# Optimization experiments

Hardware: AMD Instinct MI355X
Metric: run time of the kernel (lower is better)

Reference implementation:

```python
import jax, jax.numpy as jnp
import numpy as np
from jax.scipy.linalg import solve_triangular

EPS = 1e-5
CHUNK = 64

def _rms(x, w, eps=EPS):
    return x * jax.lax.rsqrt(jnp.mean(x * x, axis=-1, keepdims=True) + eps) * w

def _l2norm(x, eps=1e-6):
    return x * jax.lax.rsqrt(jnp.sum(x * x, axis=-1, keepdims=True) + eps)

def _causal_conv(x, w):
    # x: [B,T,C], w: [C,K] depthwise causal short conv
    K = w.shape[1]
    T = x.shape[1]
    xp = jnp.pad(x, ((0, 0), (K - 1, 0), (0, 0)))
    return sum(xp[:, j:j + T, :] * w[:, j] for j in range(K))

def _chunk_gated_delta_rule(q, k, v, g, beta, chunk=CHUNK):
    # q,k: [B,H,T,Dk] (l2-normalized, q pre-scaled); v: [B,H,T,Dv]; g,beta: [B,H,T]
    Bb, H, T, Dk = k.shape
    Dv = v.shape[-1]
    N = T // chunk
    qc, kc, vc = (a.reshape(Bb, H, N, chunk, -1) for a in (q, k, v))
    gc = g.reshape(Bb, H, N, chunk)
    bc = beta.reshape(Bb, H, N, chunk)
    gcs = jnp.cumsum(gc, axis=-1)  # within-chunk cumulative log-decay
    tri = jnp.tril(jnp.ones((chunk, chunk), bool))
    tri_s = jnp.tril(jnp.ones((chunk, chunk), bool), -1)
    diff = gcs[..., :, None] - gcs[..., None, :]
    decay = jnp.where(tri, jnp.exp(jnp.where(tri, diff, 0.0)), 0.0)  # [B,H,N,C,C]
    k_beta = kc * bc[..., None]
    v_beta = vc * bc[..., None]
    A = jnp.einsum('bhnck,bhndk->bhncd', k_beta, kc) * decay
    A = jnp.where(tri_s, A, 0.0)
    eye = jnp.eye(chunk, dtype=q.dtype)
    Tmat = solve_triangular(eye + A, jnp.broadcast_to(eye, A.shape), lower=True)  # (I+A)^-1
    u = Tmat @ v_beta                               # [B,H,N,C,Dv]
    w = Tmat @ (k_beta * jnp.exp(gcs)[..., None])   # [B,H,N,C,Dk]

    def step(S, inp):
        q_i, k_i, u_i, w_i, g_i, dm_i = inp
        attn = jnp.where(tri, jnp.einsum('bhck,bhdk->bhcd', q_i, k_i) * dm_i, 0.0)
        v_new = u_i - w_i @ S
        o_i = (q_i * jnp.exp(g_i)[..., None]) @ S + attn @ v_new
        g_last = g_i[..., -1]
        k_dec = k_i * jnp.exp(g_last[..., None] - g_i)[..., None]
        S = S * jnp.exp(g_last)[..., None, None] + jnp.einsum('bhck,bhcv->bhkv', k_dec, v_new)
        return S, o_i

    xs = tuple(jnp.moveaxis(a, 2, 0) for a in (qc, kc, u, w, gcs, decay))
    S0 = jnp.zeros((Bb, H, Dk, Dv), q.dtype)
    _, outs = jax.lax.scan(step, S0, xs)  # [N,B,H,C,Dv]
    return jnp.moveaxis(outs, 0, 2).reshape(Bb, H, T, Dv)

def _layer_forward(x, mask, ln1_w, qkvz_w, ba_w, conv_w, A_log, dt_bias,
                   o_norm_w, out_w, ln2_w, gate_w, up_w, down_w):
    B, T, D = x.shape
    H = A_log.shape[0]
    kd = qkvz_w.shape[0] // 4  # key_dim == value_dim here (k_heads==v_heads, Dk==Dv)
    vd = kd
    Dk = kd // H
    Dv = vd // H
    silu = jax.nn.silu
    h = _rms(x, ln1_w)
    qkvz = h @ qkvz_w.T
    q, k, v, z = jnp.split(qkvz, [kd, 2 * kd, 2 * kd + vd], axis=-1)
    b, a = jnp.split(h @ ba_w.T, 2, axis=-1)  # [B,T,H] each
    mixed = jnp.concatenate([q, k, v], axis=-1) * mask[..., None]
    mixed = silu(_causal_conv(mixed, conv_w))
    q, k, v = jnp.split(mixed, [kd, 2 * kd], axis=-1)
    q = _l2norm(q.reshape(B, T, H, Dk))
    k = _l2norm(k.reshape(B, T, H, Dk))
    v = v.reshape(B, T, H, Dv)
    beta = jax.nn.sigmoid(b) * mask[..., None]
    g = -jnp.exp(A_log) * jax.nn.softplus(a + dt_bias) * mask[..., None]
    scale = Dk ** -0.5
    bhtd = lambda t: jnp.transpose(t, (0, 2, 1, 3))
    o = _chunk_gated_delta_rule(bhtd(q) * scale, bhtd(k), bhtd(v),
                                jnp.transpose(g, (0, 2, 1)), jnp.transpose(beta, (0, 2, 1)))
    o = jnp.transpose(o, (0, 2, 1, 3))  # [B,T,H,Dv]
    o = _rms(o, o_norm_w) * silu(z.reshape(B, T, H, Dv))  # gated RMSNorm
    x = x + o.reshape(B, T, vd) @ out_w.T
    h2 = _rms(x, ln2_w)
    mlp_out = (silu(h2 @ gate_w.T) * (h2 @ up_w.T)) @ down_w.T
    return x + mlp_out

def setup_inputs():
    key = jax.random.key(0)
    ks = jax.random.split(key, 12)
    B, T, D, H, Dk, Dv, M, K = 1, 4096, 2048, 16, 128, 128, 8192, 4
    kd, vd = H * Dk, H * Dv
    nrm = lambda i, shp, sc=0.02: jax.random.normal(ks[i], shp, jnp.float32) * sc
    return {
        'x': nrm(0, (B, T, D), 1.0),
        'mask': jnp.ones((B, T), jnp.float32),
        'ln1_w': jnp.ones((D,), jnp.float32),
        'qkvz_w': nrm(1, (2 * kd + 2 * vd, D)),
        'ba_w': nrm(2, (2 * H, D)),
        'conv_w': nrm(3, (2 * kd + vd, K), 0.3),
        'A_log': jnp.log(jax.random.uniform(ks[4], (H,), jnp.float32, 1.0, 16.0)),
        'dt_bias': nrm(5, (H,), 0.5),
        'o_norm_w': jnp.ones((Dv,), jnp.float32),
        'out_w': nrm(6, (D, vd)),
        'ln2_w': jnp.ones((D,), jnp.float32),
        'gate_w': nrm(7, (M, D)),
        'up_w': nrm(8, (M, D)),
        'down_w': nrm(9, (D, M)),
    }

def reference(x, mask, ln1_w, qkvz_w, ba_w, conv_w, A_log, dt_bias,
              o_norm_w, out_w, ln2_w, gate_w, up_w, down_w):
    return _layer_forward(x, mask, ln1_w, qkvz_w, ba_w, conv_w, A_log, dt_bias,
                          o_norm_w, out_w, ln2_w, gate_w, up_w, down_w)
```

## Files before the change

kernel.cpp:

```cpp
#include <hip/hip_runtime.h>
#include <math.h>

#define T_LEN 4096
#define DMODEL 2048
#define NH 16
#define CQKV 6144
#define CQKVZ 8192
#define SCALE 0.08838834764831845f

using bf16x8 = __attribute__((ext_vector_type(8))) short;
using f32x4  = __attribute__((ext_vector_type(4))) float;

__device__ __forceinline__ float siluf(float x) { return x / (1.0f + __expf(-x)); }

__device__ __forceinline__ unsigned short f2bf(float f) {
  unsigned int u = __float_as_uint(f);
  u = (u + 0x7FFFu + ((u >> 16) & 1u)) >> 16;
  return (unsigned short)u;
}
__device__ __forceinline__ float bf2f(unsigned short u) {
  return __uint_as_float(((unsigned int)u) << 16);
}
__device__ __forceinline__ ushort4 pack4(float a, float b, float c, float d) {
  ushort4 r; r.x = f2bf(a); r.y = f2bf(b); r.z = f2bf(c); r.w = f2bf(d); return r;
}

__device__ __forceinline__ void gl_lds16(const unsigned short* g, unsigned short* l) {
  __builtin_amdgcn_global_load_lds(
      (const __attribute__((address_space(1))) void*)g,
      (__attribute__((address_space(3))) void*)l, 16, 0, 0);
}

template<int MODE>
__global__ __launch_bounds__(256) void rmsnorm_kernel(const float* __restrict__ x,
                                                      const float* __restrict__ w,
                                                      float* __restrict__ outf,
                                                      unsigned short* __restrict__ outb) {
  const int t = blockIdx.x;
  const int tid = threadIdx.x;
  const float4* xr = (const float4*)(x + (size_t)t * DMODEL);
  float4 v0 = xr[tid];
  float4 v1 = xr[tid + 256];
  float s = v0.x*v0.x + v0.y*v0.y + v0.z*v0.z + v0.w*v0.w
          + v1.x*v1.x + v1.y*v1.y + v1.z*v1.z + v1.w*v1.w;
#pragma unroll
  for (int off = 32; off > 0; off >>= 1) s += __shfl_down(s, off);
  __shared__ float red[4];
  if ((tid & 63) == 0) red[tid >> 6] = s;
  __syncthreads();
  const float tot = red[0] + red[1] + red[2] + red[3];
  const float r = rsqrtf(tot * (1.0f / DMODEL) + 1e-5f);
  const float4* wr = (const float4*)w;
  const float4 w0 = wr[tid], w1 = wr[tid + 256];
  float4 o0, o1;
  o0.x = v0.x*r*w0.x; o0.y = v0.y*r*w0.y; o0.z = v0.z*r*w0.z; o0.w = v0.w*r*w0.w;
  o1.x = v1.x*r*w1.x; o1.y = v1.y*r*w1.y; o1.z = v1.z*r*w1.z; o1.w = v1.w*r*w1.w;
  if (MODE == 1) {
    float4* orow = (float4*)(outf + (size_t)t * DMODEL);
    orow[tid] = o0;
    orow[tid + 256] = o1;
  }
  ushort4* brow = (ushort4*)(outb + (size_t)t * DMODEL);
  brow[tid] = pack4(o0.x, o0.y, o0.z, o0.w);
  brow[tid + 256] = pack4(o1.x, o1.y, o1.z, o1.w);
}

__global__ __launch_bounds__(256) void f2b_kernel(const float* __restrict__ in,
                                                  unsigned short* __restrict__ out) {
  const size_t i = (size_t)blockIdx.x * 256 + threadIdx.x;
  const float4 a = ((const float4*)in)[2 * i];
  const float4 b = ((const float4*)in)[2 * i + 1];
  ((ushort4*)out)[2 * i] = pack4(a.x, a.y, a.z, a.w);
  ((ushort4*)out)[2 * i + 1] = pack4(b.x, b.y, b.z, b.w);
}

template<int EPI, int BM>
__global__ __launch_bounds__(512, 1) void gemm256_kernel(const unsigned short* __restrict__ A,
                                                         const unsigned short* __restrict__ B,
                                                         float* __restrict__ Cf,
                                                         unsigned short* __restrict__ Cb,
                                                         int M, int N, int K) {
  constexpr int BN = 256;
  constexpr int MI = BM / 32;
  constexpr int AW = BM / 128;
  __shared__ __align__(16) unsigned short lds[3][(BM + BN) * 32];
  const int nbm = M / BM, nbn = N / BN, nwg = nbm * nbn;
  const int nt = K >> 5;
  int bmi, bni;
  {
    const int bid = blockIdx.x;
    const int cpx = nwg >> 3;
    int sc = 1;
    while (sc * sc < cpx) sc <<= 1;
    if (sc * sc > cpx) sc >>= 1;
    const int scn = (sc > 0) ? (cpx / sc) : 0;
    if ((nwg & 7) == 0 && sc > 0 && sc * scn == cpx && (nbm % sc) == 0 && (nbn % scn) == 0) {
      const int chunk = bid & 7, widx = bid >> 3;
      const int regc = nbn / scn;
      bmi = (chunk / regc) * sc + widx / scn;
      bni = (chunk % regc) * scn + widx % scn;
    } else {
      bmi = bid / nbn; bni = bid % nbn;
    }
  }
  const int bm = bmi * BM, bn = bni * BN;
  const int tid = threadIdx.x;
  const int wv = tid >> 6, ln = tid & 63;
  const int fr = ln & 15, qq = ln >> 4;
  const int wm = wv >> 2, wn = wv & 3;
  const int ra0 = wm * (BM / 2), rb0 = wn * 64;
  const int lrow = ln >> 2;
  const int lslot = ln & 3;

  f32x4 acc[MI][4];
  const f32x4 zero = {0.f, 0.f, 0.f, 0.f};
#pragma unroll
  for (int mi = 0; mi < MI; mi++)
#pragma unroll
    for (int ni = 0; ni < 4; ni++) acc[mi][ni] = zero;

  auto stageA = [&](int buf, int t) {
    const int k0 = t << 5;
#pragma unroll
    for (int q = 0; q < AW; q++) {
      const int lr = q * 128 + wv * 16 + lrow;
      const int sl = lslot ^ ((lr >> 1) & 3);
      gl_lds16(A + (size_t)(bm + lr) * K + k0 + sl * 8,
               &lds[buf][(q * 128 + wv * 16) * 32]);
    }
  };
  auto stageB = [&](int buf, int t) {
    const int k0 = t << 5;
#pragma unroll
    for (int q = 0; q < 2; q++) {
      const int lr = q * 128 + wv * 16 + lrow;
      const int sl = lslot ^ ((lr >> 1) & 3);
      gl_lds16(B + (size_t)(bn + lr) * K + k0 + sl * 8,
               &lds[buf][BM * 32 + (q * 128 + wv * 16) * 32]);
    }
  };

  stageA(0, 0); stageB(0, 0);
  stageA(1, 1); stageB(1, 1);
  if constexpr (AW == 2) asm volatile("s_waitcnt vmcnt(4)" ::: "memory");
  else                   asm volatile("s_waitcnt vmcnt(3)" ::: "memory");
  __builtin_amdgcn_s_barrier();
  asm volatile("" ::: "memory");

  for (int t = 0; t < nt; t++) {
    const int cb = t % 3;
    const int b2 = (t + 2) % 3;
    const unsigned short* lA = &lds[cb][0];
    const unsigned short* lB = &lds[cb][BM * 32];
    bf16x8 bfr[4];
#pragma unroll
    for (int ni = 0; ni < 4; ni++) {
      const int r = rb0 + ni * 16 + fr;
      bfr[ni] = *(const bf16x8*)&lB[r * 32 + ((qq ^ ((r >> 1) & 3)) << 3)];
    }
    bf16x8 afr[MI];
#pragma unroll
    for (int mi = 0; mi < MI; mi++) {
      const int r = ra0 + mi * 16 + fr;
      afr[mi] = *(const bf16x8*)&lA[r * 32 + ((qq ^ ((r >> 1) & 3)) << 3)];
    }
    if (t + 2 < nt) { stageA(b2, t + 2); stageB(b2, t + 2); }
    __builtin_amdgcn_s_setprio(1);
#pragma unroll
    for (int mi = 0; mi < MI; mi++)
#pragma unroll
      for (int ni = 0; ni < 4; ni++)
        acc[mi][ni] = __builtin_amdgcn_mfma_f32_16x16x32_bf16(afr[mi], bfr[ni], acc[mi][ni], 0, 0, 0);
    __builtin_amdgcn_s_setprio(0);
    if (t + 1 < nt) {
      asm volatile("s_waitcnt lgkmcnt(0)" ::: "memory");
      if (t + 2 < nt) {
        if constexpr (AW == 2) asm volatile("s_waitcnt vmcnt(4)" ::: "memory");
        else                   asm volatile("s_waitcnt vmcnt(3)" ::: "memory");
      } else {
        asm volatile("s_waitcnt vmcnt(0)" ::: "memory");
      }
      __builtin_amdgcn_s_barrier();
      asm volatile("" ::: "memory");
    }
  }

  const int cm4 = qq * 4;
#pragma unroll
  for (int mi = 0; mi < MI; mi++) {
#pragma unroll
    for (int ni = 0; ni < 4; ni++) {
#pragma unroll
      for (int r = 0; r < 4; r++) {
        const int grow = bm + ra0 + mi * 16 + cm4 + r;
        const int gcol = bn + rb0 + ni * 16 + fr;
        const size_t off = (size_t)grow * N + gcol;
        const float v = acc[mi][ni][r];
        if (EPI == 0) {
          Cb[off] = f2bf(v);
        } else if (EPI == 1) {
          Cf[off] += v;
        } else {
          Cb[off] = f2bf(siluf(bf2f(Cb[off])) * v);
        }
      }
    }
  }
}

__global__ __launch_bounds__(256) void ba_gemm_kernel(const float* __restrict__ h_in,
                                                      const float* __restrict__ ba_w,
                                                      float* __restrict__ ba_out) {
  __shared__ __align__(16) float hl[2048];
  __shared__ float red[32][9];
  const int t = blockIdx.x;
  const int tid = threadIdx.x;
  const float4* hr = (const float4*)(h_in + (size_t)t * DMODEL);
  ((float4*)hl)[tid] = hr[tid];
  ((float4*)hl)[tid + 256] = hr[tid + 256];
  __syncthreads();
  const int c = tid & 31;
  const int p = tid >> 5;
  const float* wrow = ba_w + (size_t)c * DMODEL + p * 256;
  const float* hrow = hl + p * 256;
  float s = 0.f;
#pragma unroll 8
  for (int k = 0; k < 256; k++) s += hrow[k] * wrow[k];
  red[c][p] = s;
  __syncthreads();
  if (tid < 32) {
    float tot = 0.f;
#pragma unroll
    for (int q = 0; q < 8; q++) tot += red[tid][q];
    ba_out[(size_t)t * 32 + tid] = tot;
  }
}

__global__ __launch_bounds__(256) void zcopy_kernel(const unsigned short* __restrict__ qkvz,
                                                    unsigned short* __restrict__ z) {
  const int idx = blockIdx.x * 256 + threadIdx.x;
  const int t = idx >> 8;
  const int c8 = (idx & 255) * 8;
  *(uint4*)(z + (size_t)t * 2048 + c8) =
      *(const uint4*)(qkvz + (size_t)t * CQKVZ + CQKV + c8);
}

__global__ __launch_bounds__(256) void conv_silu_kernel(const unsigned short* __restrict__ qkvz,
                                                        const float* __restrict__ conv_w,
                                                        const float* __restrict__ mask,
                                                        float* __restrict__ mixed) {
  const int idx = blockIdx.x * 256 + threadIdx.x;
  const int c4 = (idx % 1536) * 4;
  const int t = idx / 1536;
  const float4 w0 = *(const float4*)(conv_w + (size_t)c4 * 4);
  const float4 w1 = *(const float4*)(conv_w + (size_t)c4 * 4 + 4);
  const float4 w2 = *(const float4*)(conv_w + (size_t)c4 * 4 + 8);
  const float4 w3 = *(const float4*)(conv_w + (size_t)c4 * 4 + 12);
  const float wj0[4] = {w0.x, w0.y, w0.z, w0.w};
  const float wj1[4] = {w1.x, w1.y, w1.z, w1.w};
  const float wj2[4] = {w2.x, w2.y, w2.z, w2.w};
  const float wj3[4] = {w3.x, w3.y, w3.z, w3.w};
  float4 acc = make_float4(0.f, 0.f, 0.f, 0.f);
#pragma unroll
  for (int j = 0; j < 4; j++) {
    const int tt = t - 3 + j;
    if (tt < 0) continue;
    const float m = mask[tt];
    const ushort4 xb = *(const ushort4*)(qkvz + (size_t)tt * CQKVZ + c4);
    acc.x += bf2f(xb.x) * m * wj0[j];
    acc.y += bf2f(xb.y) * m * wj1[j];
    acc.z += bf2f(xb.z) * m * wj2[j];
    acc.w += bf2f(xb.w) * m * wj3[j];
  }
  acc.x = siluf(acc.x); acc.y = siluf(acc.y); acc.z = siluf(acc.z); acc.w = siluf(acc.w);
  *(float4*)(mixed + (size_t)t * CQKV + c4) = acc;
}

__global__ __launch_bounds__(256) void l2norm_kernel(float* __restrict__ mixed) {
  const int r = blockIdx.x * 4 + (threadIdx.x >> 6);
  const int lane = threadIdx.x & 63;
  const int t = r >> 5;
  const int hh = r & 31;
  float* p = mixed + (size_t)t * CQKV + hh * 128 + lane * 2;
  float2 v = *(float2*)p;
  float s = v.x * v.x + v.y * v.y;
#pragma unroll
  for (int off = 32; off > 0; off >>= 1) s += __shfl_down(s, off);
  s = __shfl(s, 0);
  const float rn = rsqrtf(s + 1e-6f);
  v.x *= rn; v.y *= rn;
  *(float2*)p = v;
}

__global__ __launch_bounds__(256) void beta_g_kernel(const float* __restrict__ ba,
                                                     const float* __restrict__ A_log,
                                                     const float* __restrict__ dt_bias,
                                                     const float* __restrict__ mask,
                                                     float* __restrict__ beta,
                                                     float* __restrict__ g) {
  const int idx = blockIdx.x * 256 + threadIdx.x;
  const int t = idx >> 4;
  const int h = idx & 15;
  const float b = ba[(size_t)t * 32 + h];
  const float a = ba[(size_t)t * 32 + 16 + h];
  const float m = mask[t];
  beta[idx] = m / (1.0f + expf(-b));
  const float xx = a + dt_bias[h];
  const float sp = (xx > 20.0f) ? xx : log1pf(expf(xx));
  g[idx] = -expf(A_log[h]) * sp * m;
}

__global__ __launch_bounds__(256) void gcs_kernel(const float* __restrict__ g,
                                                  float* __restrict__ gcsbuf,
                                                  float* __restrict__ edkbuf,
                                                  float* __restrict__ egqbuf,
                                                  float* __restrict__ adecbuf) {
  const int idx = blockIdx.x * 256 + threadIdx.x;
  if (idx >= 1024) return;
  const int h = idx >> 6;
  const int n = idx & 63;
  const int t0 = n * 64;
  float s = 0.f;
  for (int i = 0; i < 64; i++) {
    s += g[(size_t)(t0 + i) * NH + h];
    gcsbuf[(size_t)idx * 64 + i] = s;
  }
  const float glast = s;
  adecbuf[idx] = __expf(glast);
  for (int i = 0; i < 64; i++) {
    const float gi = gcsbuf[(size_t)idx * 64 + i];
    edkbuf[(size_t)idx * 64 + i] = __expf(glast - gi);
    egqbuf[(size_t)idx * 64 + i] = __expf(gi) * SCALE;
  }
}

__global__ __launch_bounds__(256) void pre_attn_kernel(const float* __restrict__ mixed,
                                                       const float* __restrict__ gcsbuf,
                                                       const float* __restrict__ betabuf,
                                                       float* __restrict__ abuf,
                                                       float* __restrict__ attnbuf) {
  __shared__ __align__(16) float kl[64][132];
  __shared__ float gcs_s[64];
  __shared__ float betal[64];
  const int blk = blockIdx.x;
  const int h = blk >> 6;
  const int n = blk & 63;
  const int t0 = n * 64;
  const int tid = threadIdx.x;
  if (tid < 64) {
    gcs_s[tid] = gcsbuf[(size_t)blk * 64 + tid];
    betal[tid] = betabuf[(size_t)(t0 + tid) * NH + h];
  }
#pragma unroll
  for (int rep = 0; rep < 8; rep++) {
    const int lin = rep * 256 + tid;
    const int i = lin >> 5;
    const int d = (lin & 31) * 4;
    const float4 kv = *(const float4*)(mixed + (size_t)(t0 + i) * CQKV + 2048 + h * 128 + d);
    *(float4*)&kl[i][d] = kv;
  }
  __syncthreads();
  const int cj = tid & 15;
  const int ri = tid >> 4;
  const int i0 = ri * 4, j0 = cj * 4;
  float accA[4][4], accQ[4][4];
#pragma unroll
  for (int a = 0; a < 4; a++)
#pragma unroll
    for (int b = 0; b < 4; b++) { accA[a][b] = 0.f; accQ[a][b] = 0.f; }
  const float* qbase = mixed + (size_t)t0 * CQKV + h * 128;
#pragma unroll 4
  for (int d = 0; d < 128; d++) {
    const float kj0 = kl[j0][d], kj1 = kl[j0 + 1][d], kj2 = kl[j0 + 2][d], kj3 = kl[j0 + 3][d];
#pragma unroll
    for (int a = 0; a < 4; a++) {
      const float ka = kl[i0 + a][d];
      const float qa = qbase[(size_t)(i0 + a) * CQKV + d];
      accA[a][0] += ka * kj0; accA[a][1] += ka * kj1; accA[a][2] += ka * kj2; accA[a][3] += ka * kj3;
      accQ[a][0] += qa * kj0; accQ[a][1] += qa * kj1; accQ[a][2] += qa * kj2; accQ[a][3] += qa * kj3;
    }
  }
#pragma unroll
  for (int a = 0; a < 4; a++) {
    const int i = i0 + a;
    const float gi = gcs_s[i];
    const float bi = betal[i];
    float4 Av, Qv;
    float dec;
    dec = __expf(fminf(gi - gcs_s[j0 + 0], 0.f));
    Av.x = (i > j0 + 0) ? accA[a][0] * bi * dec : 0.f;
    Qv.x = (i >= j0 + 0) ? accQ[a][0] * dec * SCALE : 0.f;
    dec = __expf(fminf(gi - gcs_s[j0 + 1], 0.f));
    Av.y = (i > j0 + 1) ? accA[a][1] * bi * dec : 0.f;
    Qv.y = (i >= j0 + 1) ? accQ[a][1] * dec * SCALE : 0.f;
    dec = __expf(fminf(gi - gcs_s[j0 + 2], 0.f));
    Av.z = (i > j0 + 2) ? accA[a][2] * bi * dec : 0.f;
    Qv.z = (i >= j0 + 2) ? accQ[a][2] * dec * SCALE : 0.f;
    dec = __expf(fminf(gi - gcs_s[j0 + 3], 0.f));
    Av.w = (i > j0 + 3) ? accA[a][3] * bi * dec : 0.f;
    Qv.w = (i >= j0 + 3) ? accQ[a][3] * dec * SCALE : 0.f;
    *(float4*)(abuf + (size_t)blk * 4096 + i * 64 + j0) = Av;
    *(float4*)(attnbuf + (size_t)blk * 4096 + i * 64 + j0) = Qv;
  }
}

__global__ __launch_bounds__(256) void pre_solve_kernel(const float* __restrict__ abuf,
                                                        const float* __restrict__ betabuf,
                                                        float* __restrict__ tbuf) {
  __shared__ float Al[64][65];
  __shared__ float Tl[64][65];
  const int blk = blockIdx.x;
  const int h = blk >> 6;
  const int n = blk & 63;
  const int t0 = n * 64;
  const int tid = threadIdx.x;
#pragma unroll
  for (int rep = 0; rep < 4; rep++) {
    const int lin = rep * 256 + tid;
    const int i = lin >> 4;
    const int j = (lin & 15) * 4;
    const float4 av = *(const float4*)(abuf + (size_t)blk * 4096 + i * 64 + j);
    Al[i][j] = av.x; Al[i][j + 1] = av.y; Al[i][j + 2] = av.z; Al[i][j + 3] = av.w;
  }
  __syncthreads();
  if (tid < 64) {
    const int j = tid;
    const float bj = betabuf[(size_t)(t0 + j) * NH + h];
    for (int i = 0; i < 64; i++) {
      float s = (i == j) ? 1.0f : 0.0f;
      for (int l = j; l < i; l++) s -= Al[i][l] * Tl[l][j];
      Tl[i][j] = s;
    }
    for (int i = j; i < 64; i++) Tl[i][j] *= bj;
  }
  __syncthreads();
#pragma unroll
  for (int rep = 0; rep < 4; rep++) {
    const int lin = rep * 256 + tid;
    const int i = lin >> 4;
    const int j = (lin & 15) * 4;
    float4 tv;
    tv.x = Tl[i][j]; tv.y = Tl[i][j + 1]; tv.z = Tl[i][j + 2]; tv.w = Tl[i][j + 3];
    *(float4*)(tbuf + (size_t)blk * 4096 + i * 64 + j) = tv;
  }
}

__global__ __launch_bounds__(256) void pre_uw_kernel(const float* __restrict__ mixed,
                                                     const float* __restrict__ tbuf,
                                                     const float* __restrict__ gcsbuf,
                                                     float* __restrict__ ubuf,
                                                     unsigned short* __restrict__ wbf) {
  __shared__ __align__(16) float Tl[64][68];
  __shared__ __align__(16) float xl[64][132];
  __shared__ float egcs[64];
  const int blk = blockIdx.x;
  const int h = blk >> 6;
  const int n = blk & 63;
  const int t0 = n * 64;
  const int tid = threadIdx.x;
  if (tid < 64) egcs[tid] = __expf(gcsbuf[(size_t)blk * 64 + tid]);
#pragma unroll
  for (int rep = 0; rep < 4; rep++) {
    const int lin = rep * 256 + tid;
    const int i = lin >> 4;
    const int j = (lin & 15) * 4;
    const float4 tv = *(const float4*)(tbuf + (size_t)blk * 4096 + i * 64 + j);
    *(float4*)&Tl[i][j] = tv;
  }
#pragma unroll
  for (int rep = 0; rep < 8; rep++) {
    const int lin = rep * 256 + tid;
    const int i = lin >> 5;
    const int d = (lin & 31) * 4;
    const float4 vv = *(const float4*)(mixed + (size_t)(t0 + i) * CQKV + 4096 + h * 128 + d);
    *(float4*)&xl[i][d] = vv;
  }
  __syncthreads();
  const int cgu = tid & 15;
  const int riu = tid >> 4;
  const int i0 = riu * 4;
  const int d0 = cgu * 8;
  float acc[4][8];
#pragma unroll
  for (int a = 0; a < 4; a++)
#pragma unroll
    for (int b = 0; b < 8; b++) acc[a][b] = 0.f;
#pragma unroll 2
  for (int j = 0; j < 64; j++) {
    const float tv[4] = {Tl[i0][j], Tl[i0 + 1][j], Tl[i0 + 2][j], Tl[i0 + 3][j]};
    const float4 x0 = *(const float4*)&xl[j][d0];
    const float4 x1 = *(const float4*)&xl[j][d0 + 4];
    const float xv[8] = {x0.x, x0.y, x0.z, x0.w, x1.x, x1.y, x1.z, x1.w};
#pragma unroll
    for (int a = 0; a < 4; a++)
#pragma unroll
      for (int b = 0; b < 8; b++) acc[a][b] += tv[a] * xv[b];
  }
#pragma unroll
  for (int b = 0; b < 8; b++) {
    *(float4*)(ubuf + (size_t)blk * 8192 + riu * 512 + (size_t)(d0 + b) * 4) =
        make_float4(acc[0][b], acc[1][b], acc[2][b], acc[3][b]);
  }
  __syncthreads();
#pragma unroll
  for (int rep = 0; rep < 8; rep++) {
    const int lin = rep * 256 + tid;
    const int i = lin >> 5;
    const int d = (lin & 31) * 4;
    float4 kv = *(const float4*)(mixed + (size_t)(t0 + i) * CQKV + 2048 + h * 128 + d);
    const float e = egcs[i];
    kv.x *= e; kv.y *= e; kv.z *= e; kv.w *= e;
    *(float4*)&xl[i][d] = kv;
  }
  __syncthreads();
#pragma unroll
  for (int a = 0; a < 4; a++)
#pragma unroll
    for (int b = 0; b < 8; b++) acc[a][b] = 0.f;
#pragma unroll 2
  for (int j = 0; j < 64; j++) {
    const float tv[4] = {Tl[i0][j], Tl[i0 + 1][j], Tl[i0 + 2][j], Tl[i0 + 3][j]};
    const float4 x0 = *(const float4*)&xl[j][d0];
    const float4 x1 = *(const float4*)&xl[j][d0 + 4];
    const float xv[8] = {x0.x, x0.y, x0.z, x0.w, x1.x, x1.y, x1.z, x1.w};
#pragma unroll
    for (int a = 0; a < 4; a++)
#pragma unroll
      for (int b = 0; b < 8; b++) acc[a][b] += tv[a] * xv[b];
  }
#pragma unroll
  for (int a = 0; a < 4; a++) {
    const int l = i0 + a;
    unsigned short* wp = wbf + (size_t)(t0 + l) * 2048 + h * 128 + ((cgu ^ (l & 7)) << 3);
    *(ushort4*)wp = pack4(-acc[a][0], -acc[a][1], -acc[a][2], -acc[a][3]);
    *(ushort4*)(wp + 4) = pack4(-acc[a][4], -acc[a][5], -acc[a][6], -acc[a][7]);
  }
}

__global__ __launch_bounds__(256) void ktrans_kernel(const float* __restrict__ mixed,
                                                     const float* __restrict__ edkbuf,
                                                     const float* __restrict__ egqbuf,
                                                     unsigned short* __restrict__ kdT,
                                                     unsigned short* __restrict__ qe) {
  __shared__ __align__(16) float kl[64][132];
  __shared__ float edk_s[64];
  __shared__ float egq_s[64];
  const int blk = blockIdx.x;
  const int h = blk >> 6;
  const int n = blk & 63;
  const int t0 = n * 64;
  const int tid = threadIdx.x;
  if (tid < 64) {
    edk_s[tid] = edkbuf[(size_t)blk * 64 + tid];
    egq_s[tid] = egqbuf[(size_t)blk * 64 + tid];
  }
#pragma unroll
  for (int q = 0; q < 8; q++) {
    const int idx = tid + q * 256;
    const int l = idx >> 5, c4 = (idx & 31) * 4;
    *(float4*)&kl[l][c4] = *(const float4*)(mixed + (size_t)(t0 + l) * CQKV + 2048 + h * 128 + c4);
  }
  __syncthreads();
#pragma unroll
  for (int q = 0; q < 4; q++) {
    const int idx = tid + q * 256;
    const int d = idx >> 3, lsl = idx & 7;
    const int l8 = lsl * 8;
    float v[8];
#pragma unroll
    for (int j = 0; j < 8; j++) v[j] = kl[l8 + j][d] * edk_s[l8 + j];
    unsigned short* p = kdT + (size_t)blk * 8192 + d * 64 + ((lsl ^ (d & 7)) << 3);
    *(ushort4*)p = pack4(v[0], v[1], v[2], v[3]);
    *(ushort4*)(p + 4) = pack4(v[4], v[5], v[6], v[7]);
  }
#pragma unroll
  for (int q = 0; q < 8; q++) {
    const int idx = tid + q * 256;
    const int i = idx >> 5, c4 = (idx & 31) * 4;
    const float4 v = *(const float4*)(mixed + (size_t)(t0 + i) * CQKV + h * 128 + c4);
    const float e = egq_s[i];
    *(ushort4*)(qe + (size_t)(t0 + i) * 2048 + h * 128 + c4) =
        pack4(v.x * e, v.y * e, v.z * e, v.w * e);
  }
}

__global__ __launch_bounds__(512, 1) void scan_kernel(const unsigned short* __restrict__ wbf,
                                                      const unsigned short* __restrict__ kdT,
                                                      const float* __restrict__ ubuf,
                                                      const float* __restrict__ adecbuf,
                                                      unsigned short* __restrict__ STb,
                                                      unsigned short* __restrict__ vtb,
                                                      const float* __restrict__ gw,
                                                      const float* __restrict__ uw,
                                                      const float* __restrict__ dw,
                                                      const float* __restrict__ ow,
                                                      const float* __restrict__ xin,
                                                      unsigned short* __restrict__ Wg,
                                                      unsigned short* __restrict__ Wu,
                                                      unsigned short* __restrict__ Wd,
                                                      unsigned short* __restrict__ Wo,
                                                      float* __restrict__ outc) {
  __shared__ __align__(16) unsigned short stage[2][16384];
  __shared__ __align__(16) unsigned short privAll[8][3072];
  if (blockIdx.x >= 16) {
    const int xb = blockIdx.x - 16;
    const int tid = threadIdx.x;
    if (xb < 13312) {
      const float* src; unsigned short* dst; size_t u;
      if (xb < 4096)       { src = gw; dst = Wg; u = (size_t)xb * 512 + tid; }
      else if (xb < 8192)  { src = uw; dst = Wu; u = (size_t)(xb - 4096) * 512 + tid; }
      else if (xb < 12288) { src = dw; dst = Wd; u = (size_t)(xb - 8192) * 512 + tid; }
      else                 { src = ow; dst = Wo; u = (size_t)(xb - 12288) * 512 + tid; }
      const float4 a = ((const float4*)src)[2 * u];
      const float4 b = ((const float4*)src)[2 * u + 1];
      ((ushort4*)dst)[2 * u] = pack4(a.x, a.y, a.z, a.w);
      ((ushort4*)dst)[2 * u + 1] = pack4(b.x, b.y, b.z, b.w);
    } else {
      const size_t i = (size_t)(xb - 13312) * 512 + tid;
      ((float4*)outc)[2 * i] = ((const float4*)xin)[2 * i];
      ((float4*)outc)[2 * i + 1] = ((const float4*)xin)[2 * i + 1];
    }
    return;
  }
  const int h = blockIdx.x;
  const int tid = threadIdx.x;
  const int ln = tid & 63;
  const int wv = tid >> 6;
  const int fr = ln & 15;
  const int g  = ln >> 4;
  const int c0 = wv * 16;
  const int fsw = fr & 7;
  unsigned short* privA = &privAll[wv][0];
  unsigned short* privB = &privAll[wv][2048];
  const f32x4 zero = {0.f, 0.f, 0.f, 0.f};

  f32x4 acc2[8];
#pragma unroll
  for (int dt = 0; dt < 8; dt++) acc2[dt] = zero;

  auto stage_wk = [&](int buf, int n1) {
    const int t0n = n1 * 64;
    const size_t kbase = (size_t)(h * 64 + n1) * 8192;
#pragma unroll
    for (int q = 0; q < 2; q++) {
      const int m = wv * 2 + q;
      gl_lds16(wbf + (size_t)(t0n + m * 4 + (ln >> 4)) * 2048 + h * 128 + (ln & 15) * 8,
               &stage[buf][m * 512]);
      gl_lds16(kdT + kbase + (m * 8 + (ln >> 3)) * 64 + (ln & 7) * 8,
               &stage[buf][8192 + m * 512]);
    }
  };

  float4 ur4[4];
#pragma unroll
  for (int lt = 0; lt < 4; lt++)
    ur4[lt] = *(const float4*)(ubuf + (size_t)(h * 64) * 8192 + (lt * 4 + g) * 512 + (c0 + fr) * 4);
  float ad = adecbuf[h * 64];
  stage_wk(0, 0);
  asm volatile("s_waitcnt vmcnt(0)" ::: "memory");
  __builtin_amdgcn_s_barrier();
  asm volatile("" ::: "memory");

  for (int n = 0; n < 64; n++) {
    const int blk = h * 64 + n;
    const unsigned short* wl = &stage[n & 1][0];
    const unsigned short* kl = &stage[n & 1][8192];
    if (n + 1 < 64) stage_wk((n + 1) & 1, n + 1);
    __builtin_amdgcn_sched_barrier(0);
    float4 ur4n[4];
    float adn = 0.f;
    if (n + 1 < 64) {
      const size_t ub = (size_t)(blk + 1) * 8192;
#pragma unroll
      for (int lt = 0; lt < 4; lt++)
        ur4n[lt] = *(const float4*)(ubuf + ub + (lt * 4 + g) * 512 + (c0 + fr) * 4);
      adn = adecbuf[blk + 1];
    } else {
      const float4 z4 = make_float4(0.f, 0.f, 0.f, 0.f);
#pragma unroll
      for (int lt = 0; lt < 4; lt++) ur4n[lt] = z4;
    }
    __builtin_amdgcn_sched_barrier(0);
#pragma unroll
    for (int dt = 0; dt < 8; dt++) {
      const int slot = dt * 2 + (g >> 1);
      const ushort4 pv = pack4(acc2[dt][0], acc2[dt][1], acc2[dt][2], acc2[dt][3]);
      *(ushort4*)&privA[fr * 128 + ((slot ^ fsw) << 3) + (g & 1) * 4] = pv;
      *(ushort4*)(STb + (size_t)blk * 16384 + (dt * 4 + g) * 512 + (c0 + fr) * 4) = pv;
    }
    f32x4 acc1[4];
#pragma unroll
    for (int lt = 0; lt < 4; lt++) {
      f32x4 t;
      t[0] = ur4[lt].x; t[1] = ur4[lt].y; t[2] = ur4[lt].z; t[3] = ur4[lt].w;
      acc1[lt] = t;
    }
#pragma unroll
    for (int ks = 0; ks < 4; ks++) {
      const int kb = ks * 4 + g;
      const bf16x8 b = *(const bf16x8*)&privA[fr * 128 + ((kb ^ fsw) << 3)];
#pragma unroll
      for (int lt = 0; lt < 4; lt++) {
        const bf16x8 a = *(const bf16x8*)&wl[(lt * 16 + fr) * 128 + ((kb ^ fsw) << 3)];
        acc1[lt] = __builtin_amdgcn_mfma_f32_16x16x32_bf16(a, b, acc1[lt], 0, 0, 0);
      }
    }
#pragma unroll
    for (int lt = 0; lt < 4; lt++) {
      const int slot = lt * 2 + (g >> 1);
      const ushort4 pv = pack4(acc1[lt][0], acc1[lt][1], acc1[lt][2], acc1[lt][3]);
      *(ushort4*)&privB[fr * 64 + ((slot ^ fsw) << 3) + (g & 1) * 4] = pv;
      *(ushort4*)(vtb + (size_t)blk * 8192 + (lt * 4 + g) * 512 + (c0 + fr) * 4) = pv;
    }
#pragma unroll
    for (int dt = 0; dt < 8; dt++) {
      acc2[dt][0] *= ad; acc2[dt][1] *= ad; acc2[dt][2] *= ad; acc2[dt][3] *= ad;
    }
#pragma unroll
    for (int ks = 0; ks < 2; ks++) {
      const int kb = ks * 4 + g;
      const bf16x8 b = *(const bf16x8*)&privB[fr * 64 + ((kb ^ fsw) << 3)];
#pragma unroll
      for (int dt = 0; dt < 8; dt++) {
        const bf16x8 a = *(const bf16x8*)&kl[(dt * 16 + fr) * 64 + ((kb ^ fsw) << 3)];
        acc2[dt] = __builtin_amdgcn_mfma_f32_16x16x32_bf16(a, b, acc2[dt], 0, 0, 0);
      }
    }
#pragma unroll
    for (int lt = 0; lt < 4; lt++) ur4[lt] = ur4n[lt];
    ad = adn;
    if (n + 1 < 64) {
      asm volatile("s_waitcnt lgkmcnt(0)" ::: "memory");
      __builtin_amdgcn_sched_barrier(0);
      asm volatile("s_waitcnt vmcnt(17)" ::: "memory");
      __builtin_amdgcn_sched_barrier(0);
      __builtin_amdgcn_s_barrier();
      __builtin_amdgcn_sched_barrier(0);
    }
  }
}

__global__ __launch_bounds__(256) void ocomp_kernel(const unsigned short* __restrict__ qe,
                                                    const unsigned short* __restrict__ STbuf,
                                                    const unsigned short* __restrict__ vtbuf,
                                                    const float* __restrict__ attnbuf,
                                                    const unsigned short* __restrict__ zb,
                                                    const float* __restrict__ onw,
                                                    unsigned short* __restrict__ ob) {
  __shared__ __align__(16) unsigned short STl[128 * 128];
  __shared__ __align__(16) unsigned short vtl[128 * 64];
  __shared__ __align__(16) unsigned short ql[64 * 128];
  __shared__ __align__(16) unsigned short al[64 * 64];
  const int blk = blockIdx.x;
  const int h = blk >> 6;
  const int n = blk & 63;
  const int t0 = n * 64;
  const int tid = threadIdx.x;
#pragma unroll
  for (int q = 0; q < 8; q++) {
    const int o = tid + q * 256;
    const int dq = o >> 6, w = o & 63;
    const uint4 v = *(const uint4*)(STbuf + (size_t)blk * 16384 + (size_t)o * 8);
    const int cA = 2 * w, cB = 2 * w + 1;
    const int base = ((dq >> 1)) ;
    uint2 h0; h0.x = v.x; h0.y = v.y;
    uint2 h1; h1.x = v.z; h1.y = v.w;
    *(uint2*)&STl[cA * 128 + (((dq >> 1) ^ (cA & 7)) << 3) + (dq & 1) * 4] = h0;
    *(uint2*)&STl[cB * 128 + (((dq >> 1) ^ (cB & 7)) << 3) + (dq & 1) * 4] = h1;
    (void)base;
  }
#pragma unroll
  for (int q = 0; q < 4; q++) {
    const int o = tid + q * 256;
    const int lq = o >> 6, w = o & 63;
    const uint4 v = *(const uint4*)(vtbuf + (size_t)blk * 8192 + (size_t)o * 8);
    const int cA = 2 * w, cB = 2 * w + 1;
    uint2 h0; h0.x = v.x; h0.y = v.y;
    uint2 h1; h1.x = v.z; h1.y = v.w;
    *(uint2*)&vtl[cA * 64 + (((lq >> 1) ^ (cA & 7)) << 3) + (lq & 1) * 4] = h0;
    *(uint2*)&vtl[cB * 64 + (((lq >> 1) ^ (cB & 7)) << 3) + (lq & 1) * 4] = h1;
  }
#pragma unroll
  for (int q = 0; q < 4; q++) {
    const int idx = tid + q * 256;
    const int i = idx >> 4, dg = idx & 15;
    *(uint4*)&ql[i * 128 + ((dg ^ (i & 7)) << 3)] =
        *(const uint4*)(qe + (size_t)(t0 + i) * 2048 + h * 128 + dg * 8);
  }
#pragma unroll
  for (int q = 0; q < 4; q++) {
    const int idx = tid + q * 256;
    const int i = idx >> 4, l4 = (idx & 15) * 4;
    const float4 v = *(const float4*)(attnbuf + (size_t)blk * 4096 + i * 64 + l4);
    *(ushort4*)&al[i * 64 + (((l4 >> 3) ^ (i & 7)) << 3) + (l4 & 7)] =
        pack4(v.x, v.y, v.z, v.w);
  }
  __syncthreads();
  const int ln = tid & 63;
  const int wv = tid >> 6;
  const int fr = ln & 15;
  const int g = ln >> 4;
  const int i0 = wv * 16;
  f32x4 acc[8];
  const f32x4 zero = {0.f, 0.f, 0.f, 0.f};
#pragma unroll
  for (int nt = 0; nt < 8; nt++) acc[nt] = zero;
#pragma unroll
  for (int ks = 0; ks < 4; ks++) {
    const int kb = ks * 4 + g;
    const int ar = i0 + fr;
    const bf16x8 a = *(const bf16x8*)&ql[ar * 128 + ((kb ^ (ar & 7)) << 3)];
#pragma unroll
    for (int nt = 0; nt < 8; nt++) {
      const int c = nt * 16 + fr;
      const bf16x8 b = *(const bf16x8*)&STl[c * 128 + ((kb ^ (c & 7)) << 3)];
      acc[nt] = __builtin_amdgcn_mfma_f32_16x16x32_bf16(a, b, acc[nt], 0, 0, 0);
    }
  }
#pragma unroll
  for (int ks = 0; ks < 2; ks++) {
    const int kb = ks * 4 + g;
    const int ar = i0 + fr;
    const bf16x8 a = *(const bf16x8*)&al[ar * 64 + ((kb ^ (ar & 7)) << 3)];
#pragma unroll
    for (int nt = 0; nt < 8; nt++) {
      const int c = nt * 16 + fr;
      const bf16x8 b = *(const bf16x8*)&vtl[c * 64 + ((kb ^ (c & 7)) << 3)];
      acc[nt] = __builtin_amdgcn_mfma_f32_16x16x32_bf16(a, b, acc[nt], 0, 0, 0);
    }
  }
  float s0 = 0.f, s1 = 0.f, s2 = 0.f, s3 = 0.f;
#pragma unroll
  for (int nt = 0; nt < 8; nt++) {
    s0 += acc[nt][0] * acc[nt][0];
    s1 += acc[nt][1] * acc[nt][1];
    s2 += acc[nt][2] * acc[nt][2];
    s3 += acc[nt][3] * acc[nt][3];
  }
#pragma unroll
  for (int m = 1; m < 16; m <<= 1) {
    s0 += __shfl_xor(s0, m);
    s1 += __shfl_xor(s1, m);
    s2 += __shfl_xor(s2, m);
    s3 += __shfl_xor(s3, m);
  }
  float rn[4];
  rn[0] = rsqrtf(s0 * (1.0f / 128.0f) + 1e-5f);
  rn[1] = rsqrtf(s1 * (1.0f / 128.0f) + 1e-5f);
  rn[2] = rsqrtf(s2 * (1.0f / 128.0f) + 1e-5f);
  rn[3] = rsqrtf(s3 * (1.0f / 128.0f) + 1e-5f);
#pragma unroll
  for (int nt = 0; nt < 8; nt++) {
    const int c = nt * 16 + fr;
    const float wn = onw[c];
#pragma unroll
    for (int r = 0; r < 4; r++) {
      const size_t off = (size_t)(t0 + i0 + g * 4 + r) * 2048 + h * 128 + c;
      const float zz = siluf(bf2f(zb[off]));
      ob[off] = f2bf(acc[nt][r] * rn[r] * wn * zz);
    }
  }
}

extern "C" void kernel_launch(void* const* d_in, const int* in_sizes, int n_in,
                              void* d_out, int out_size, void* d_ws, size_t ws_size,
                              hipStream_t stream) {
  (void)in_sizes; (void)n_in; (void)out_size;
  const float* x        = (const float*)d_in[0];
  const float* mask     = (const float*)d_in[1];
  const float* ln1_w    = (const float*)d_in[2];
  const float* qkvz_w   = (const float*)d_in[3];
  const float* ba_w     = (const float*)d_in[4];
  const float* conv_w   = (const float*)d_in[5];
  const float* A_log    = (const float*)d_in[6];
  const float* dt_bias  = (const float*)d_in[7];
  const float* o_norm_w = (const float*)d_in[8];
  const float* out_w    = (const float*)d_in[9];
  const float* ln2_w    = (const float*)d_in[10];
  const float* gate_w   = (const float*)d_in[11];
  const float* up_w     = (const float*)d_in[12];
  const float* down_w   = (const float*)d_in[13];
  float* out = (float*)d_out;

  const size_t NEED_BYTES = (size_t)75825152 * 4;
  if (ws_size < NEED_BYTES) return;

  float* ws = (float*)d_ws;
  float* mixed_buf = ws;
  unsigned short* Wg = (unsigned short*)ws;
  unsigned short* Wu = (unsigned short*)(ws + 8388608);
  unsigned short* Wd = (unsigned short*)(ws + 16777216);
  unsigned short* qkvz_bf = (unsigned short*)(ws + 25165824);
  float* u_buf = ws + 25165824;
  unsigned short* wbf = (unsigned short*)(ws + 33554432);
  unsigned short* kdT = (unsigned short*)(ws + 37748736);
  unsigned short* gate_bf = (unsigned short*)(ws + 25165824);
  unsigned short* z_bf = (unsigned short*)(ws + 41943040);
  float* h_buf = ws + 46137344;
  float* a_buf = ws + 46137344;
  unsigned short* vt_buf = (unsigned short*)(ws + 46137344);
  float* t_buf = ws + 50331648;
  unsigned short* qe_bf = (unsigned short*)(ws + 50331648);
  unsigned short* h_bf  = (unsigned short*)(ws + 54525952);
  unsigned short* ob    = (unsigned short*)(ws + 54525952);
  unsigned short* h2_bf = (unsigned short*)(ws + 54525952);
  float* attn_buf = ws + 58720256;
  unsigned short* Wq = (unsigned short*)(ws + 62914560);
  unsigned short* ST_buf = (unsigned short*)(ws + 62914560);
  unsigned short* Wo = (unsigned short*)(ws + 71303168);
  float* ba_buf   = ws + 73400320;
  float* beta_buf = ws + 73531392;
  float* g_buf    = ws + 73596928;
  float* gcs_buf  = ws + 73662464;
  float* edk_buf  = ws + 73728000;
  float* egq_buf  = ws + 73793536;
  float* adec_buf = ws + 73859072;

  rmsnorm_kernel<1><<<4096, 256, 0, stream>>>(x, ln1_w, h_buf, h_bf);
  f2b_kernel<<<8192, 256, 0, stream>>>(qkvz_w, Wq);
  gemm256_kernel<0, 256><<<512, 512, 0, stream>>>(h_bf, Wq, nullptr, qkvz_bf, 4096, 8192, 2048);
  ba_gemm_kernel<<<4096, 256, 0, stream>>>(h_buf, ba_w, ba_buf);
  zcopy_kernel<<<4096, 256, 0, stream>>>(qkvz_bf, z_bf);
  conv_silu_kernel<<<24576, 256, 0, stream>>>(qkvz_bf, conv_w, mask, mixed_buf);
  l2norm_kernel<<<32768, 256, 0, stream>>>(mixed_buf);
  beta_g_kernel<<<256, 256, 0, stream>>>(ba_buf, A_log, dt_bias, mask, beta_buf, g_buf);
  gcs_kernel<<<4, 256, 0, stream>>>(g_buf, gcs_buf, edk_buf, egq_buf, adec_buf);
  pre_attn_kernel<<<1024, 256, 0, stream>>>(mixed_buf, gcs_buf, beta_buf, a_buf, attn_buf);
  pre_solve_kernel<<<1024, 256, 0, stream>>>(a_buf, beta_buf, t_buf);
  pre_uw_kernel<<<1024, 256, 0, stream>>>(mixed_buf, t_buf, gcs_buf, u_buf, wbf);
  ktrans_kernel<<<1024, 256, 0, stream>>>(mixed_buf, edk_buf, egq_buf, kdT, qe_bf);
  scan_kernel<<<15376, 512, 0, stream>>>(wbf, kdT, u_buf, adec_buf, ST_buf, vt_buf,
                                         gate_w, up_w, down_w, out_w, x,
                                         Wg, Wu, Wd, Wo, out);
  ocomp_kernel<<<1024, 256, 0, stream>>>(qe_bf, ST_buf, vt_buf, attn_buf,
                                         z_bf, o_norm_w, ob);
  gemm256_kernel<1, 128><<<256, 512, 0, stream>>>(ob, Wo, out, nullptr, 4096, 2048, 2048);
  rmsnorm_kernel<2><<<4096, 256, 0, stream>>>(out, ln2_w, nullptr, h2_bf);
  gemm256_kernel<0, 256><<<512, 512, 0, stream>>>(h2_bf, Wg, nullptr, gate_bf, 4096, 8192, 2048);
  gemm256_kernel<2, 256><<<512, 512, 0, stream>>>(h2_bf, Wu, nullptr, gate_bf, 4096, 8192, 2048);
  gemm256_kernel<1, 128><<<256, 512, 0, stream>>>(gate_bf, Wd, out, nullptr, 4096, 2048, 8192);
}
```

Baseline: 1.372 ms.

## Shrink GEMM tiles, switch to double buffering, raise occupancy launch bounds

The GEMM kernel is now templated on BN and uses smaller tiles (128x256 for the large projections, 128x128 for the down and out projections), launching twice as many workgroups. The LDS pipeline drops from triple to double buffering with a full vmcnt(0) wait every iteration. Launch bounds are raised to allow up to 4 workgroups per CU, so latency is hidden by occupancy rather than deeper prefetch. The trade-off is less data reuse per tile and a less overlapped load pipeline.

```diff
diff --git a/kernel.cpp b/kernel.cpp
--- a/kernel.cpp
+++ b/kernel.cpp
@@ -74,16 +74,17 @@
   ((ushort4*)out)[2 * i + 1] = pack4(b.x, b.y, b.z, b.w);
 }
 
-template<int EPI, int BM>
-__global__ __launch_bounds__(512, 1) void gemm256_kernel(const unsigned short* __restrict__ A,
+template<int EPI, int BM, int BN>
+__global__ __launch_bounds__(512, 4) void gemm256_kernel(const unsigned short* __restrict__ A,
                                                          const unsigned short* __restrict__ B,
                                                          float* __restrict__ Cf,
                                                          unsigned short* __restrict__ Cb,
                                                          int M, int N, int K) {
-  constexpr int BN = 256;
-  constexpr int MI = BM / 32;
+  constexpr int MI = 4;
+  constexpr int NI = BN / 64;
   constexpr int AW = BM / 128;
-  __shared__ __align__(16) unsigned short lds[3][(BM + BN) * 32];
+  constexpr int BW = BN / 128;
+  __shared__ __align__(16) unsigned short lds[2][(BM + BN) * 32];
   const int nbm = M / BM, nbn = N / BN, nwg = nbm * nbn;
   const int nt = K >> 5;
   int bmi, bni;
@@ -108,18 +109,18 @@
   const int wv = tid >> 6, ln = tid & 63;
   const int fr = ln & 15, qq = ln >> 4;
   const int wm = wv >> 2, wn = wv & 3;
-  const int ra0 = wm * (BM / 2), rb0 = wn * 64;
+  const int ra0 = wm * 64, rb0 = wn * (BN / 4);
   const int lrow = ln >> 2;
   const int lslot = ln & 3;
 
-  f32x4 acc[MI][4];
+  f32x4 acc[MI][NI];
   const f32x4 zero = {0.f, 0.f, 0.f, 0.f};
 #pragma unroll
   for (int mi = 0; mi < MI; mi++)
 #pragma unroll
-    for (int ni = 0; ni < 4; ni++) acc[mi][ni] = zero;
-
-  auto stageA = [&](int buf, int t) {
+    for (int ni = 0; ni < NI; ni++) acc[mi][ni] = zero;
+
+  auto stage = [&](int buf, int t) {
     const int k0 = t << 5;
 #pragma unroll
     for (int q = 0; q < AW; q++) {
@@ -128,11 +129,8 @@
       gl_lds16(A + (size_t)(bm + lr) * K + k0 + sl * 8,
                &lds[buf][(q * 128 + wv * 16) * 32]);
     }
-  };
-  auto stageB = [&](int buf, int t) {
-    const int k0 = t << 5;
-#pragma unroll
-    for (int q = 0; q < 2; q++) {
+#pragma unroll
+    for (int q = 0; q < BW; q++) {
       const int lr = q * 128 + wv * 16 + lrow;
       const int sl = lslot ^ ((lr >> 1) & 3);
       gl_lds16(B + (size_t)(bn + lr) * K + k0 + sl * 8,
@@ -140,21 +138,18 @@
     }
   };
 
-  stageA(0, 0); stageB(0, 0);
-  stageA(1, 1); stageB(1, 1);
-  if constexpr (AW == 2) asm volatile("s_waitcnt vmcnt(4)" ::: "memory");
-  else                   asm volatile("s_waitcnt vmcnt(3)" ::: "memory");
+  stage(0, 0);
+  asm volatile("s_waitcnt vmcnt(0)" ::: "memory");
   __builtin_amdgcn_s_barrier();
   asm volatile("" ::: "memory");
 
   for (int t = 0; t < nt; t++) {
-    const int cb = t % 3;
-    const int b2 = (t + 2) % 3;
-    const unsigned short* lA = &lds[cb][0];
-    const unsigned short* lB = &lds[cb][BM * 32];
-    bf16x8 bfr[4];
-#pragma unroll
-    for (int ni = 0; ni < 4; ni++) {
+    if (t + 1 < nt) stage((t + 1) & 1, t + 1);
+    const unsigned short* lA = &lds[t & 1][0];
+    const unsigned short* lB = &lds[t & 1][BM * 32];
+    bf16x8 bfr[NI];
+#pragma unroll
+    for (int ni = 0; ni < NI; ni++) {
       const int r = rb0 + ni * 16 + fr;
       bfr[ni] = *(const bf16x8*)&lB[r * 32 + ((qq ^ ((r >> 1) & 3)) << 3)];
     }
@@ -164,22 +159,16 @@
       const int r = ra0 + mi * 16 + fr;
       afr[mi] = *(const bf16x8*)&lA[r * 32 + ((qq ^ ((r >> 1) & 3)) << 3)];
     }
-    if (t + 2 < nt) { stageA(b2, t + 2); stageB(b2, t + 2); }
     __builtin_amdgcn_s_setprio(1);
 #pragma unroll
     for (int mi = 0; mi < MI; mi++)
 #pragma unroll
-      for (int ni = 0; ni < 4; ni++)
+      for (int ni = 0; ni < NI; ni++)
         acc[mi][ni] = __builtin_amdgcn_mfma_f32_16x16x32_bf16(afr[mi], bfr[ni], acc[mi][ni], 0, 0, 0);
     __builtin_amdgcn_s_setprio(0);
     if (t + 1 < nt) {
       asm volatile("s_waitcnt lgkmcnt(0)" ::: "memory");
-      if (t + 2 < nt) {
-        if constexpr (AW == 2) asm volatile("s_waitcnt vmcnt(4)" ::: "memory");
-        else                   asm volatile("s_waitcnt vmcnt(3)" ::: "memory");
-      } else {
-        asm volatile("s_waitcnt vmcnt(0)" ::: "memory");
-      }
+      asm volatile("s_waitcnt vmcnt(0)" ::: "memory");
       __builtin_amdgcn_s_barrier();
       asm volatile("" ::: "memory");
     }
@@ -189,7 +178,7 @@
 #pragma unroll
   for (int mi = 0; mi < MI; mi++) {
 #pragma unroll
-    for (int ni = 0; ni < 4; ni++) {
+    for (int ni = 0; ni < NI; ni++) {
 #pragma unroll
       for (int r = 0; r < 4; r++) {
         const int grow = bm + ra0 + mi * 16 + cm4 + r;
@@ -762,12 +751,10 @@
     const int dq = o >> 6, w = o & 63;
     const uint4 v = *(const uint4*)(STbuf + (size_t)blk * 16384 + (size_t)o * 8);
     const int cA = 2 * w, cB = 2 * w + 1;
-    const int base = ((dq >> 1)) ;
     uint2 h0; h0.x = v.x; h0.y = v.y;
     uint2 h1; h1.x = v.z; h1.y = v.w;
     *(uint2*)&STl[cA * 128 + (((dq >> 1) ^ (cA & 7)) << 3) + (dq & 1) * 4] = h0;
     *(uint2*)&STl[cB * 128 + (((dq >> 1) ^ (cB & 7)) << 3) + (dq & 1) * 4] = h1;
-    (void)base;
   }
 #pragma unroll
   for (int q = 0; q < 4; q++) {
@@ -918,7 +905,7 @@
 
   rmsnorm_kernel<1><<<4096, 256, 0, stream>>>(x, ln1_w, h_buf, h_bf);
   f2b_kernel<<<8192, 256, 0, stream>>>(qkvz_w, Wq);
-  gemm256_kernel<0, 256><<<512, 512, 0, stream>>>(h_bf, Wq, nullptr, qkvz_bf, 4096, 8192, 2048);
+  gemm256_kernel<0, 128, 256><<<1024, 512, 0, stream>>>(h_bf, Wq, nullptr, qkvz_bf, 4096, 8192, 2048);
   ba_gemm_kernel<<<4096, 256, 0, stream>>>(h_buf, ba_w, ba_buf);
   zcopy_kernel<<<4096, 256, 0, stream>>>(qkvz_bf, z_bf);
   conv_silu_kernel<<<24576, 256, 0, stream>>>(qkvz_bf, conv_w, mask, mixed_buf);
@@ -934,9 +921,9 @@
                                          Wg, Wu, Wd, Wo, out);
   ocomp_kernel<<<1024, 256, 0, stream>>>(qe_bf, ST_buf, vt_buf, attn_buf,
                                          z_bf, o_norm_w, ob);
-  gemm256_kernel<1, 128><<<256, 512, 0, stream>>>(ob, Wo, out, nullptr, 4096, 2048, 2048);
+  gemm256_kernel<1, 128, 128><<<512, 512, 0, stream>>>(ob, Wo, out, nullptr, 4096, 2048, 2048);
   rmsnorm_kernel<2><<<4096, 256, 0, stream>>>(out, ln2_w, nullptr, h2_bf);
-  gemm256_kernel<0, 256><<<512, 512, 0, stream>>>(h2_bf, Wg, nullptr, gate_bf, 4096, 8192, 2048);
-  gemm256_kernel<2, 256><<<512, 512, 0, stream>>>(h2_bf, Wu, nullptr, gate_bf, 4096, 8192, 2048);
-  gemm256_kernel<1, 128><<<256, 512, 0, stream>>>(gate_bf, Wd, out, nullptr, 4096, 2048, 8192);
-}
+  gemm256_kernel<0, 128, 256><<<1024, 512, 0, stream>>>(h2_bf, Wg, nullptr, gate_bf, 4096, 8192, 2048);
+  gemm256_kernel<2, 128, 256><<<1024, 512, 0, stream>>>(h2_bf, Wu, nullptr, gate_bf, 4096, 8192, 2048);
+  gemm256_kernel<1, 128, 128><<<512, 512, 0, stream>>>(gate_bf, Wd, out, nullptr, 4096, 2048, 8192);
+}
```

After: 1.381 ms. No clear change (+0.7%).
